# Performance work log

Hardware: AMD Instinct MI355X
Metric: run time of the kernel (lower is better)

Reference implementation:

```python
import jax, jax.numpy as jnp
import numpy as np


def setup_inputs() -> dict:
    key = jax.random.key(0)
    k0, k1, k2, k3 = jax.random.split(key, 4)
    B, s, D, E, H = 4, 1024, 1024, 8, 4096
    return {
        "x": jax.random.normal(k0, (B, s, D), dtype=jnp.float32),
        "gate_weight": jax.random.normal(k1, (E, D), dtype=jnp.float32) * 0.006,
        "expert_bias": jnp.zeros((E, 1), dtype=jnp.float32),
        "w1": jax.random.normal(k2, (E, D, H), dtype=jnp.float32) * 0.02,
        "b1": jnp.zeros((E, H), dtype=jnp.float32),
        "w2": jax.random.normal(k3, (E, H, D), dtype=jnp.float32) * 0.02,
        "b2": jnp.zeros((E, D), dtype=jnp.float32),
        "capacity": 2,
    }


def reference(x, gate_weight, expert_bias, w1, b1, w2, b2, capacity):
    B, s, D = x.shape
    E = gate_weight.shape[0]
    xf = x.reshape(-1, D)          # [S, D]
    S = xf.shape[0]
    k = int(S * capacity)          # number of routed (expert, token) pairs

    # Router: logits [E, S], softmax over experts (dim=0 in the torch code)
    logits = jnp.einsum('ed,sd->es', gate_weight, xf) + expert_bias
    scores = jax.nn.softmax(logits, axis=0)  # [E, S]

    # Global top-k over the flattened [E, S] score matrix (idx // S = expert,
    # idx % S = token, matching the source's index arithmetic).
    _, idx = jax.lax.top_k(scores.reshape(-1), k)
    sel = jnp.zeros((E * S,), dtype=scores.dtype).at[idx].set(1.0)
    combine = scores * sel.reshape(E, S)     # gating value where selected, else 0

    # Dense per-expert MLP on all tokens (same math as gather -> expert -> scatter,
    # expressed as masked combine). GELU(tanh approx) as in the repo's Mlp.
    h = jax.nn.gelu(jnp.einsum('sd,edh->esh', xf, w1) + b1[:, None, :],
                    approximate=True)        # [E, S, H]
    out_e = jnp.einsum('esh,ehd->esd', h, w2) + b2[:, None, :]  # [E, S, D]

    out = jnp.einsum('es,esd->sd', combine, out_e)  # scatter-combine
    return out.reshape(B, s, D)
```

## Files before the change

### kernel.cpp

```cpp
#include <hip/hip_runtime.h>
#include <stdint.h>

#define S_TOK 4096
#define DIM   1024
#define NE    8
#define HID   4096

typedef __attribute__((ext_vector_type(4))) float f32x4;
typedef __attribute__((ext_vector_type(8))) short bf16x8;

static __device__ __forceinline__ ushort f2bf(float f) {
  uint u = __float_as_uint(f);
  u += 0x7FFFu + ((u >> 16) & 1u);
  return (ushort)(u >> 16);
}

static __device__ __forceinline__ double shfl_xor_d(double v, int off) {
  long long l = __double_as_longlong(v);
  int lo = (int)(l & 0xFFFFFFFFll), hi = (int)(l >> 32);
  lo = __shfl_xor(lo, off);
  hi = __shfl_xor(hi, off);
  return __longlong_as_double(((long long)hi << 32) | (unsigned int)lo);
}

__global__ __launch_bounds__(256) void router_kernel(
    const float* __restrict__ x, const float* __restrict__ gw,
    const float* __restrict__ bias, double* __restrict__ scoresd,
    ushort* __restrict__ xb)
{
  const int t = blockIdx.x * 4 + (threadIdx.x >> 6);
  const int lane = threadIdx.x & 63;
  double acc[NE];
#pragma unroll
  for (int e = 0; e < NE; ++e) acc[e] = 0.0;
  const float4* xrow = (const float4*)(x + (size_t)t * DIM);
  ushort* xbrow = xb + (size_t)t * DIM;
#pragma unroll
  for (int j = 0; j < 4; ++j) {
    const int c4 = j * 64 + lane;
    float4 xv = xrow[c4];
    ushort4 bv;
    bv.x = f2bf(xv.x); bv.y = f2bf(xv.y); bv.z = f2bf(xv.z); bv.w = f2bf(xv.w);
    ((ushort4*)xbrow)[c4] = bv;
#pragma unroll
    for (int e = 0; e < NE; ++e) {
      float4 g = ((const float4*)(gw + (size_t)e * DIM))[c4];
      acc[e] += (double)xv.x * g.x + (double)xv.y * g.y
              + (double)xv.z * g.z + (double)xv.w * g.w;
    }
  }
#pragma unroll
  for (int e = 0; e < NE; ++e) {
    double v = acc[e];
#pragma unroll
    for (int off = 32; off >= 1; off >>= 1) v += shfl_xor_d(v, off);
    acc[e] = v + (double)bias[e];
  }
  double m = acc[0];
#pragma unroll
  for (int e = 1; e < NE; ++e) m = (acc[e] > m) ? acc[e] : m;
  double den = 0.0;
#pragma unroll
  for (int e = 0; e < NE; ++e) { acc[e] = exp(acc[e] - m); den += acc[e]; }
  const double inv = 1.0 / den;
#pragma unroll
  for (int e = 0; e < NE; ++e)
    if (lane == e) scoresd[(size_t)e * S_TOK + t] = acc[e] * inv;
}

__global__ __launch_bounds__(1024) void select_kernel(
    const double* __restrict__ scoresd, const int* __restrict__ capacity,
    int* __restrict__ counts, int* __restrict__ bases,
    int* __restrict__ lists, float* __restrict__ gates)
{
  __shared__ int sh_cnt;
  __shared__ unsigned long long sh_p;
  __shared__ int sh_r;
  __shared__ int wsum[16];
  __shared__ int sh_run;
  __shared__ int cnt_e[NE];
  const int tid = threadIdx.x, lane = tid & 63, wv = tid >> 6;
  const int k = S_TOK * capacity[0];

  unsigned long long key[32];
#pragma unroll
  for (int c = 0; c < 32; ++c)
    key[c] = (unsigned long long)__double_as_longlong(scoresd[c * 1024 + tid]);

  if (tid == 0) { sh_p = 0ull; sh_r = k; sh_run = 0; }
  if (tid < NE) cnt_e[tid] = 0;
  __syncthreads();

  for (int b = 63; b >= 0; --b) {
    if (tid == 0) sh_cnt = 0;
    __syncthreads();
    const unsigned long long p = sh_p;
    const unsigned long long mask = (~0ull) << b;
    const unsigned long long test = p | (1ull << b);
    int local = 0;
#pragma unroll
    for (int c = 0; c < 32; ++c) local += ((key[c] & mask) == test) ? 1 : 0;
#pragma unroll
    for (int off = 32; off >= 1; off >>= 1) local += __shfl_xor(local, off);
    if (lane == 0) atomicAdd(&sh_cnt, local);
    __syncthreads();
    if (tid == 0) {
      if (sh_r <= sh_cnt) sh_p |= (1ull << b); else sh_r -= sh_cnt;
    }
    __syncthreads();
  }
  const unsigned long long p = sh_p;

  if (tid == 0) sh_cnt = 0;
  __syncthreads();
  {
    int local = 0;
#pragma unroll
    for (int c = 0; c < 32; ++c) local += (key[c] > p) ? 1 : 0;
#pragma unroll
    for (int off = 32; off >= 1; off >>= 1) local += __shfl_xor(local, off);
    if (lane == 0) atomicAdd(&sh_cnt, local);
  }
  __syncthreads();
  const int need_eq = k - sh_cnt;

#pragma unroll
  for (int c = 0; c < 32; ++c) {
    const int i = c * 1024 + tid;
    const bool gt = key[c] > p;
    const bool eq = (key[c] == p);
    const unsigned long long bal = __ballot(eq);
    const int wpref = __popcll(bal & ((1ull << lane) - 1ull));
    if (lane == 0) wsum[wv] = __popcll(bal);
    __syncthreads();
    int wbase = 0;
    for (int w = 0; w < wv; ++w) wbase += wsum[w];
    const int rank = sh_run + wbase + wpref;
    if (gt || (eq && rank < need_eq)) {
      const int e = i >> 12;
      const int s = i & (S_TOK - 1);
      const int slot = atomicAdd(&cnt_e[e], 1);
      lists[e * S_TOK + slot] = s;
      gates[e * S_TOK + slot] = (float)__longlong_as_double((long long)key[c]);
    }
    __syncthreads();
    if (tid == 0) {
      int tot = 0;
      for (int w = 0; w < 16; ++w) tot += wsum[w];
      sh_run += tot;
    }
    __syncthreads();
  }

  if (tid == 0) {
    int b0 = 0;
    for (int e = 0; e < NE; ++e) { counts[e] = cnt_e[e]; bases[e] = b0; b0 += cnt_e[e]; }
  }
}

__global__ __launch_bounds__(256) void gemm1_kernel(
    const ushort* __restrict__ xb, const float* __restrict__ w1,
    const float* __restrict__ b1, const int* __restrict__ counts,
    const int* __restrict__ bases, const int* __restrict__ lists,
    ushort* __restrict__ hbuf)
{
  const int e = blockIdx.z;
  const int ne = counts[e];
  const int row0 = blockIdx.y * 128;
  if (row0 >= ne) return;
  const int n0 = blockIdx.x * 128;
  const int base = bases[e];

  __shared__ ushort Al[128 * 40];
  __shared__ ushort Bl[128 * 40];

  const int tid = threadIdx.x, lane = tid & 63, wid = tid >> 6;
  const int wm = wid >> 1, wn = wid & 1;

  const int ar0 = tid >> 2, ksa = tid & 3;
  const int tr0 = min(row0 + ar0, ne - 1);
  const int tr1 = min(row0 + 64 + ar0, ne - 1);
  const ushort* aptr0 = xb + (size_t)lists[e * S_TOK + tr0] * DIM + ksa * 8;
  const ushort* aptr1 = xb + (size_t)lists[e * S_TOK + tr1] * DIM + ksa * 8;

  const int hb = tid & 127, ksb = tid >> 7;
  const float* wb = w1 + (size_t)e * DIM * HID + (size_t)(n0 + hb);

  f32x4 acc[4][4];
#pragma unroll
  for (int i = 0; i < 4; ++i)
#pragma unroll
    for (int j = 0; j < 4; ++j) acc[i][j] = (f32x4){0.f, 0.f, 0.f, 0.f};

  for (int kk = 0; kk < DIM; kk += 32) {
    int4 av0 = *(const int4*)(aptr0 + kk);
    int4 av1 = *(const int4*)(aptr1 + kk);
    float fa[8], fbv[8];
#pragma unroll
    for (int j = 0; j < 8; ++j) {
      fa[j]  = wb[(size_t)(kk + ksb * 8 + j) * HID];
      fbv[j] = wb[(size_t)(kk + (ksb + 2) * 8 + j) * HID];
    }
    union { ushort u[8]; int4 v; } p0, p1;
#pragma unroll
    for (int j = 0; j < 8; ++j) { p0.u[j] = f2bf(fa[j]); p1.u[j] = f2bf(fbv[j]); }
    __syncthreads();
    *(int4*)&Al[ar0 * 40 + ksa * 8] = av0;
    *(int4*)&Al[(64 + ar0) * 40 + ksa * 8] = av1;
    *(int4*)&Bl[hb * 40 + ksb * 8] = p0.v;
    *(int4*)&Bl[hb * 40 + (ksb + 2) * 8] = p1.v;
    __syncthreads();
    bf16x8 af[4], bf[4];
#pragma unroll
    for (int m = 0; m < 4; ++m)
      af[m] = *(const bf16x8*)&Al[(wm * 64 + m * 16 + (lane & 15)) * 40 + (lane >> 4) * 8];
#pragma unroll
    for (int n = 0; n < 4; ++n)
      bf[n] = *(const bf16x8*)&Bl[(wn * 64 + n * 16 + (lane & 15)) * 40 + (lane >> 4) * 8];
#pragma unroll
    for (int m = 0; m < 4; ++m)
#pragma unroll
      for (int n = 0; n < 4; ++n)
        acc[m][n] = __builtin_amdgcn_mfma_f32_16x16x32_bf16(af[m], bf[n], acc[m][n], 0, 0, 0);
  }

  const float* b1e = b1 + (size_t)e * HID + n0;
#pragma unroll
  for (int m = 0; m < 4; ++m) {
#pragma unroll
    for (int r = 0; r < 4; ++r) {
      const int row = wm * 64 + m * 16 + (lane >> 4) * 4 + r;
      if (row0 + row < ne) {
        const size_t hrow = (size_t)(base + row0 + row) * HID + n0;
#pragma unroll
        for (int n = 0; n < 4; ++n) {
          const int col = wn * 64 + n * 16 + (lane & 15);
          float v = acc[m][n][r] + b1e[col];
          float t = v + 0.044715f * v * v * v;
          float g = v / (1.0f + __expf(-1.5957691216f * t));
          hbuf[hrow + col] = f2bf(g);
        }
      }
    }
  }
}

__global__ __launch_bounds__(256) void gemm2_kernel(
    const ushort* __restrict__ hbuf, const float* __restrict__ w2,
    const float* __restrict__ b2, const int* __restrict__ counts,
    const int* __restrict__ bases, const int* __restrict__ lists,
    const float* __restrict__ gates, float* __restrict__ out)
{
  const int e = blockIdx.z;
  const int ne = counts[e];
  const int row0 = blockIdx.y * 128;
  if (row0 >= ne) return;
  const int n0 = blockIdx.x * 128;
  const int base = bases[e];

  __shared__ ushort Al[128 * 40];
  __shared__ ushort Bl[128 * 40];

  const int tid = threadIdx.x, lane = tid & 63, wid = tid >> 6;
  const int wm = wid >> 1, wn = wid & 1;

  const int ar0 = tid >> 2, ksa = tid & 3;
  const size_t hr0 = (size_t)(base + min(row0 + ar0, ne - 1)) * HID;
  const size_t hr1 = (size_t)(base + min(row0 + 64 + ar0, ne - 1)) * HID;
  const ushort* aptr0 = hbuf + hr0 + ksa * 8;
  const ushort* aptr1 = hbuf + hr1 + ksa * 8;

  const int hb = tid & 127, ksb = tid >> 7;
  const float* wb = w2 + (size_t)e * HID * DIM + (size_t)(n0 + hb);

  f32x4 acc[4][4];
#pragma unroll
  for (int i = 0; i < 4; ++i)
#pragma unroll
    for (int j = 0; j < 4; ++j) acc[i][j] = (f32x4){0.f, 0.f, 0.f, 0.f};

  for (int kk = 0; kk < HID; kk += 32) {
    int4 av0 = *(const int4*)(aptr0 + kk);
    int4 av1 = *(const int4*)(aptr1 + kk);
    float fa[8], fbv[8];
#pragma unroll
    for (int j = 0; j < 8; ++j) {
      fa[j]  = wb[(size_t)(kk + ksb * 8 + j) * DIM];
      fbv[j] = wb[(size_t)(kk + (ksb + 2) * 8 + j) * DIM];
    }
    union { ushort u[8]; int4 v; } p0, p1;
#pragma unroll
    for (int j = 0; j < 8; ++j) { p0.u[j] = f2bf(fa[j]); p1.u[j] = f2bf(fbv[j]); }
    __syncthreads();
    *(int4*)&Al[ar0 * 40 + ksa * 8] = av0;
    *(int4*)&Al[(64 + ar0) * 40 + ksa * 8] = av1;
    *(int4*)&Bl[hb * 40 + ksb * 8] = p0.v;
    *(int4*)&Bl[hb * 40 + (ksb + 2) * 8] = p1.v;
    __syncthreads();
    bf16x8 af[4], bf[4];
#pragma unroll
    for (int m = 0; m < 4; ++m)
      af[m] = *(const bf16x8*)&Al[(wm * 64 + m * 16 + (lane & 15)) * 40 + (lane >> 4) * 8];
#pragma unroll
    for (int n = 0; n < 4; ++n)
      bf[n] = *(const bf16x8*)&Bl[(wn * 64 + n * 16 + (lane & 15)) * 40 + (lane >> 4) * 8];
#pragma unroll
    for (int m = 0; m < 4; ++m)
#pragma unroll
      for (int n = 0; n < 4; ++n)
        acc[m][n] = __builtin_amdgcn_mfma_f32_16x16x32_bf16(af[m], bf[n], acc[m][n], 0, 0, 0);
  }

  const float* b2e = b2 + (size_t)e * DIM + n0;
#pragma unroll
  for (int m = 0; m < 4; ++m) {
#pragma unroll
    for (int r = 0; r < 4; ++r) {
      const int row = wm * 64 + m * 16 + (lane >> 4) * 4 + r;
      if (row0 + row < ne) {
        const int tok = lists[e * S_TOK + row0 + row];
        const float gv = gates[e * S_TOK + row0 + row];
        float* orow = out + (size_t)tok * DIM + n0;
#pragma unroll
        for (int n = 0; n < 4; ++n) {
          const int col = wn * 64 + n * 16 + (lane & 15);
          const float v = gv * (acc[m][n][r] + b2e[col]);
          __hip_atomic_fetch_add(&orow[col], v, __ATOMIC_RELAXED, __HIP_MEMORY_SCOPE_AGENT);
        }
      }
    }
  }
}

extern "C" void kernel_launch(void* const* d_in, const int* in_sizes, int n_in,
                              void* d_out, int out_size, void* d_ws, size_t ws_size,
                              hipStream_t stream)
{
  const float* x    = (const float*)d_in[0];
  const float* gw   = (const float*)d_in[1];
  const float* bias = (const float*)d_in[2];
  const float* w1   = (const float*)d_in[3];
  const float* b1   = (const float*)d_in[4];
  const float* w2   = (const float*)d_in[5];
  const float* b2   = (const float*)d_in[6];
  const int*   cap  = (const int*)d_in[7];
  float* out = (float*)d_out;
  char* ws = (char*)d_ws;

  ushort* xb      = (ushort*)(ws);
  ushort* hbuf    = (ushort*)(ws + (size_t)8  * (1 << 20));
  double* scoresd = (double*)(ws + (size_t)72 * (1 << 20));
  int*    lists   = (int*)   (ws + (size_t)73 * (1 << 20));
  float*  gates   = (float*) (ws + (size_t)74 * (1 << 20));
  int*    counts  = (int*)   (ws + (size_t)75 * (1 << 20));
  int*    bases   = counts + 64;

  hipMemsetAsync(d_out, 0, (size_t)out_size * sizeof(float), stream);

  router_kernel<<<dim3(S_TOK / 4), 256, 0, stream>>>(x, gw, bias, scoresd, xb);
  select_kernel<<<dim3(1), 1024, 0, stream>>>(scoresd, cap, counts, bases, lists, gates);
  gemm1_kernel<<<dim3(HID / 128, 32, NE), 256, 0, stream>>>(xb, w1, b1, counts, bases, lists, hbuf);
  gemm2_kernel<<<dim3(DIM / 128, 32, NE), 256, 0, stream>>>(hbuf, w2, b2, counts, bases, lists, gates, out);
}
```

Baseline: 788.7 us.

## Pre-transpose weights to bf16 and stream tiles via global_load_lds in hidden chunks

Adds a per-call kernel that transposes and converts each expert's fp32 W1/W2 to bf16 in a K-contiguous layout. The GEMMs then load both operands with direct global-to-LDS 16-byte loads into a swizzled 32-wide LDS layout, replacing strided scalar fp32 weight loads and in-loop conversion. The hidden dimension is split into two chunks so the transposed weights and intermediate activations fit the workspace, and gemm2 accumulates each chunk atomically, adding the bias only once. The cost is extra weight-prep passes, more launches, and a second round of atomic output adds.

```diff
diff --git a/kernel.cpp b/kernel.cpp
--- a/kernel.cpp
+++ b/kernel.cpp
@@ -5,6 +5,7 @@
 #define DIM   1024
 #define NE    8
 #define HID   4096
+#define HC    2048
 
 typedef __attribute__((ext_vector_type(4))) float f32x4;
 typedef __attribute__((ext_vector_type(8))) short bf16x8;
@@ -13,6 +14,12 @@
   uint u = __float_as_uint(f);
   u += 0x7FFFu + ((u >> 16) & 1u);
   return (ushort)(u >> 16);
+}
+
+static __device__ __forceinline__ void gload16(const ushort* g, ushort* l) {
+  __builtin_amdgcn_global_load_lds(
+      (const __attribute__((address_space(1))) void*)g,
+      (__attribute__((address_space(3))) void*)l, 16, 0, 0);
 }
 
 static __device__ __forceinline__ double shfl_xor_d(double v, int off) {
@@ -21,6 +28,38 @@
   lo = __shfl_xor(lo, off);
   hi = __shfl_xor(hi, off);
   return __longlong_as_double(((long long)hi << 32) | (unsigned int)lo);
+}
+
+__global__ __launch_bounds__(256) void wprep_kernel(
+    const float* __restrict__ w, ushort* __restrict__ wT,
+    int R, int rowStride, size_t eIn, size_t eOut)
+{
+  __shared__ float tile[64][65];
+  const int e = blockIdx.z;
+  const int c0 = blockIdx.x * 64, r0 = blockIdx.y * 64;
+  const float* we = w + (size_t)e * eIn;
+  ushort* wTe = wT + (size_t)e * eOut;
+  const int t = threadIdx.x;
+  const int rr = t >> 4, cq = t & 15;
+#pragma unroll
+  for (int p = 0; p < 4; ++p) {
+    float4 v = *(const float4*)(we + (size_t)(r0 + p * 16 + rr) * rowStride + c0 + cq * 4);
+    tile[p * 16 + rr][cq * 4 + 0] = v.x;
+    tile[p * 16 + rr][cq * 4 + 1] = v.y;
+    tile[p * 16 + rr][cq * 4 + 2] = v.z;
+    tile[p * 16 + rr][cq * 4 + 3] = v.w;
+  }
+  __syncthreads();
+#pragma unroll
+  for (int p = 0; p < 4; ++p) {
+    const int cc = p * 16 + rr;
+    ushort4 o;
+    o.x = f2bf(tile[cq * 4 + 0][cc]);
+    o.y = f2bf(tile[cq * 4 + 1][cc]);
+    o.z = f2bf(tile[cq * 4 + 2][cc]);
+    o.w = f2bf(tile[cq * 4 + 3][cc]);
+    *(ushort4*)(wTe + (size_t)(c0 + cc) * R + r0 + cq * 4) = o;
+  }
 }
 
 __global__ __launch_bounds__(256) void router_kernel(
@@ -159,10 +198,10 @@
 }
 
 __global__ __launch_bounds__(256) void gemm1_kernel(
-    const ushort* __restrict__ xb, const float* __restrict__ w1,
+    const ushort* __restrict__ xb, const ushort* __restrict__ wT,
     const float* __restrict__ b1, const int* __restrict__ counts,
     const int* __restrict__ bases, const int* __restrict__ lists,
-    ushort* __restrict__ hbuf)
+    ushort* __restrict__ hbuf, int hc0)
 {
   const int e = blockIdx.z;
   const int ne = counts[e];
@@ -171,20 +210,28 @@
   const int n0 = blockIdx.x * 128;
   const int base = bases[e];
 
-  __shared__ ushort Al[128 * 40];
-  __shared__ ushort Bl[128 * 40];
-
-  const int tid = threadIdx.x, lane = tid & 63, wid = tid >> 6;
-  const int wm = wid >> 1, wn = wid & 1;
-
-  const int ar0 = tid >> 2, ksa = tid & 3;
-  const int tr0 = min(row0 + ar0, ne - 1);
-  const int tr1 = min(row0 + 64 + ar0, ne - 1);
-  const ushort* aptr0 = xb + (size_t)lists[e * S_TOK + tr0] * DIM + ksa * 8;
-  const ushort* aptr1 = xb + (size_t)lists[e * S_TOK + tr1] * DIM + ksa * 8;
-
-  const int hb = tid & 127, ksb = tid >> 7;
-  const float* wb = w1 + (size_t)e * DIM * HID + (size_t)(n0 + hb);
+  __shared__ ushort Al[128 * 32];
+  __shared__ ushort Bl[128 * 32];
+
+  const int tid = threadIdx.x, lane = tid & 63, w = tid >> 6;
+  const int wm = w >> 1, wn = w & 1;
+  const int r15 = lane & 15;
+
+  const int sr = w * 32 + (lane >> 2);
+  const int sslot = (lane & 3) ^ ((lane >> 3) & 3);
+  const int tr0 = min(row0 + sr, ne - 1);
+  const int tr1 = min(row0 + sr + 16, ne - 1);
+  const ushort* ap0 = xb + (size_t)lists[e * S_TOK + tr0] * DIM + sslot * 8;
+  const ushort* ap1 = xb + (size_t)lists[e * S_TOK + tr1] * DIM + sslot * 8;
+  const ushort* wTe = wT + (size_t)e * HC * DIM;
+  const ushort* bp0 = wTe + (size_t)(n0 + sr) * DIM + sslot * 8;
+  const ushort* bp1 = wTe + (size_t)(n0 + sr + 16) * DIM + sslot * 8;
+  ushort* la0 = &Al[w * 1024];
+  ushort* la1 = &Al[w * 1024 + 512];
+  ushort* lb0 = &Bl[w * 1024];
+  ushort* lb1 = &Bl[w * 1024 + 512];
+
+  const int slotr = ((lane >> 4) ^ ((lane >> 1) & 3)) * 8;
 
   f32x4 acc[4][4];
 #pragma unroll
@@ -193,48 +240,37 @@
     for (int j = 0; j < 4; ++j) acc[i][j] = (f32x4){0.f, 0.f, 0.f, 0.f};
 
   for (int kk = 0; kk < DIM; kk += 32) {
-    int4 av0 = *(const int4*)(aptr0 + kk);
-    int4 av1 = *(const int4*)(aptr1 + kk);
-    float fa[8], fbv[8];
-#pragma unroll
-    for (int j = 0; j < 8; ++j) {
-      fa[j]  = wb[(size_t)(kk + ksb * 8 + j) * HID];
-      fbv[j] = wb[(size_t)(kk + (ksb + 2) * 8 + j) * HID];
-    }
-    union { ushort u[8]; int4 v; } p0, p1;
-#pragma unroll
-    for (int j = 0; j < 8; ++j) { p0.u[j] = f2bf(fa[j]); p1.u[j] = f2bf(fbv[j]); }
-    __syncthreads();
-    *(int4*)&Al[ar0 * 40 + ksa * 8] = av0;
-    *(int4*)&Al[(64 + ar0) * 40 + ksa * 8] = av1;
-    *(int4*)&Bl[hb * 40 + ksb * 8] = p0.v;
-    *(int4*)&Bl[hb * 40 + (ksb + 2) * 8] = p1.v;
-    __syncthreads();
-    bf16x8 af[4], bf[4];
+    __syncthreads();
+    gload16(ap0 + kk, la0);
+    gload16(ap1 + kk, la1);
+    gload16(bp0 + kk, lb0);
+    gload16(bp1 + kk, lb1);
+    __syncthreads();
+    bf16x8 af[4], bfr[4];
 #pragma unroll
     for (int m = 0; m < 4; ++m)
-      af[m] = *(const bf16x8*)&Al[(wm * 64 + m * 16 + (lane & 15)) * 40 + (lane >> 4) * 8];
+      af[m] = *(const bf16x8*)&Al[(wm * 64 + m * 16 + r15) * 32 + slotr];
 #pragma unroll
     for (int n = 0; n < 4; ++n)
-      bf[n] = *(const bf16x8*)&Bl[(wn * 64 + n * 16 + (lane & 15)) * 40 + (lane >> 4) * 8];
+      bfr[n] = *(const bf16x8*)&Bl[(wn * 64 + n * 16 + r15) * 32 + slotr];
 #pragma unroll
     for (int m = 0; m < 4; ++m)
 #pragma unroll
       for (int n = 0; n < 4; ++n)
-        acc[m][n] = __builtin_amdgcn_mfma_f32_16x16x32_bf16(af[m], bf[n], acc[m][n], 0, 0, 0);
-  }
-
-  const float* b1e = b1 + (size_t)e * HID + n0;
+        acc[m][n] = __builtin_amdgcn_mfma_f32_16x16x32_bf16(af[m], bfr[n], acc[m][n], 0, 0, 0);
+  }
+
+  const float* b1e = b1 + (size_t)e * HID + hc0 + n0;
 #pragma unroll
   for (int m = 0; m < 4; ++m) {
 #pragma unroll
     for (int r = 0; r < 4; ++r) {
       const int row = wm * 64 + m * 16 + (lane >> 4) * 4 + r;
       if (row0 + row < ne) {
-        const size_t hrow = (size_t)(base + row0 + row) * HID + n0;
+        const size_t hrow = (size_t)(base + row0 + row) * HC + n0;
 #pragma unroll
         for (int n = 0; n < 4; ++n) {
-          const int col = wn * 64 + n * 16 + (lane & 15);
+          const int col = wn * 64 + n * 16 + r15;
           float v = acc[m][n][r] + b1e[col];
           float t = v + 0.044715f * v * v * v;
           float g = v / (1.0f + __expf(-1.5957691216f * t));
@@ -246,10 +282,10 @@
 }
 
 __global__ __launch_bounds__(256) void gemm2_kernel(
-    const ushort* __restrict__ hbuf, const float* __restrict__ w2,
+    const ushort* __restrict__ hbuf, const ushort* __restrict__ wT,
     const float* __restrict__ b2, const int* __restrict__ counts,
     const int* __restrict__ bases, const int* __restrict__ lists,
-    const float* __restrict__ gates, float* __restrict__ out)
+    const float* __restrict__ gates, float* __restrict__ out, int addBias)
 {
   const int e = blockIdx.z;
   const int ne = counts[e];
@@ -258,20 +294,28 @@
   const int n0 = blockIdx.x * 128;
   const int base = bases[e];
 
-  __shared__ ushort Al[128 * 40];
-  __shared__ ushort Bl[128 * 40];
-
-  const int tid = threadIdx.x, lane = tid & 63, wid = tid >> 6;
-  const int wm = wid >> 1, wn = wid & 1;
-
-  const int ar0 = tid >> 2, ksa = tid & 3;
-  const size_t hr0 = (size_t)(base + min(row0 + ar0, ne - 1)) * HID;
-  const size_t hr1 = (size_t)(base + min(row0 + 64 + ar0, ne - 1)) * HID;
-  const ushort* aptr0 = hbuf + hr0 + ksa * 8;
-  const ushort* aptr1 = hbuf + hr1 + ksa * 8;
-
-  const int hb = tid & 127, ksb = tid >> 7;
-  const float* wb = w2 + (size_t)e * HID * DIM + (size_t)(n0 + hb);
+  __shared__ ushort Al[128 * 32];
+  __shared__ ushort Bl[128 * 32];
+
+  const int tid = threadIdx.x, lane = tid & 63, w = tid >> 6;
+  const int wm = w >> 1, wn = w & 1;
+  const int r15 = lane & 15;
+
+  const int sr = w * 32 + (lane >> 2);
+  const int sslot = (lane & 3) ^ ((lane >> 3) & 3);
+  const int tr0 = min(row0 + sr, ne - 1);
+  const int tr1 = min(row0 + sr + 16, ne - 1);
+  const ushort* ap0 = hbuf + (size_t)(base + tr0) * HC + sslot * 8;
+  const ushort* ap1 = hbuf + (size_t)(base + tr1) * HC + sslot * 8;
+  const ushort* wTe = wT + (size_t)e * DIM * HC;
+  const ushort* bp0 = wTe + (size_t)(n0 + sr) * HC + sslot * 8;
+  const ushort* bp1 = wTe + (size_t)(n0 + sr + 16) * HC + sslot * 8;
+  ushort* la0 = &Al[w * 1024];
+  ushort* la1 = &Al[w * 1024 + 512];
+  ushort* lb0 = &Bl[w * 1024];
+  ushort* lb1 = &Bl[w * 1024 + 512];
+
+  const int slotr = ((lane >> 4) ^ ((lane >> 1) & 3)) * 8;
 
   f32x4 acc[4][4];
 #pragma unroll
@@ -279,36 +323,25 @@
 #pragma unroll
     for (int j = 0; j < 4; ++j) acc[i][j] = (f32x4){0.f, 0.f, 0.f, 0.f};
 
-  for (int kk = 0; kk < HID; kk += 32) {
-    int4 av0 = *(const int4*)(aptr0 + kk);
-    int4 av1 = *(const int4*)(aptr1 + kk);
-    float fa[8], fbv[8];
-#pragma unroll
-    for (int j = 0; j < 8; ++j) {
-      fa[j]  = wb[(size_t)(kk + ksb * 8 + j) * DIM];
-      fbv[j] = wb[(size_t)(kk + (ksb + 2) * 8 + j) * DIM];
-    }
-    union { ushort u[8]; int4 v; } p0, p1;
-#pragma unroll
-    for (int j = 0; j < 8; ++j) { p0.u[j] = f2bf(fa[j]); p1.u[j] = f2bf(fbv[j]); }
-    __syncthreads();
-    *(int4*)&Al[ar0 * 40 + ksa * 8] = av0;
-    *(int4*)&Al[(64 + ar0) * 40 + ksa * 8] = av1;
-    *(int4*)&Bl[hb * 40 + ksb * 8] = p0.v;
-    *(int4*)&Bl[hb * 40 + (ksb + 2) * 8] = p1.v;
-    __syncthreads();
-    bf16x8 af[4], bf[4];
+  for (int kk = 0; kk < HC; kk += 32) {
+    __syncthreads();
+    gload16(ap0 + kk, la0);
+    gload16(ap1 + kk, la1);
+    gload16(bp0 + kk, lb0);
+    gload16(bp1 + kk, lb1);
+    __syncthreads();
+    bf16x8 af[4], bfr[4];
 #pragma unroll
     for (int m = 0; m < 4; ++m)
-      af[m] = *(const bf16x8*)&Al[(wm * 64 + m * 16 + (lane & 15)) * 40 + (lane >> 4) * 8];
+      af[m] = *(const bf16x8*)&Al[(wm * 64 + m * 16 + r15) * 32 + slotr];
 #pragma unroll
     for (int n = 0; n < 4; ++n)
-      bf[n] = *(const bf16x8*)&Bl[(wn * 64 + n * 16 + (lane & 15)) * 40 + (lane >> 4) * 8];
+      bfr[n] = *(const bf16x8*)&Bl[(wn * 64 + n * 16 + r15) * 32 + slotr];
 #pragma unroll
     for (int m = 0; m < 4; ++m)
 #pragma unroll
       for (int n = 0; n < 4; ++n)
-        acc[m][n] = __builtin_amdgcn_mfma_f32_16x16x32_bf16(af[m], bf[n], acc[m][n], 0, 0, 0);
+        acc[m][n] = __builtin_amdgcn_mfma_f32_16x16x32_bf16(af[m], bfr[n], acc[m][n], 0, 0, 0);
   }
 
   const float* b2e = b2 + (size_t)e * DIM + n0;
@@ -323,8 +356,9 @@
         float* orow = out + (size_t)tok * DIM + n0;
 #pragma unroll
         for (int n = 0; n < 4; ++n) {
-          const int col = wn * 64 + n * 16 + (lane & 15);
-          const float v = gv * (acc[m][n][r] + b2e[col]);
+          const int col = wn * 64 + n * 16 + r15;
+          const float bb = addBias ? b2e[col] : 0.f;
+          const float v = gv * (acc[m][n][r] + bb);
           __hip_atomic_fetch_add(&orow[col], v, __ATOMIC_RELAXED, __HIP_MEMORY_SCOPE_AGENT);
         }
       }
@@ -349,16 +383,27 @@
 
   ushort* xb      = (ushort*)(ws);
   ushort* hbuf    = (ushort*)(ws + (size_t)8  * (1 << 20));
+  ushort* wT      = (ushort*)(ws + (size_t)40 * (1 << 20));
   double* scoresd = (double*)(ws + (size_t)72 * (1 << 20));
-  int*    lists   = (int*)   (ws + (size_t)73 * (1 << 20));
-  float*  gates   = (float*) (ws + (size_t)74 * (1 << 20));
-  int*    counts  = (int*)   (ws + (size_t)75 * (1 << 20));
+  int*    lists   = (int*)   (ws + (size_t)72 * (1 << 20) + 262144);
+  float*  gates   = (float*) (ws + (size_t)72 * (1 << 20) + 262144 + 131072);
+  int*    counts  = (int*)   (ws + (size_t)72 * (1 << 20) + 262144 + 262144);
   int*    bases   = counts + 64;
 
   hipMemsetAsync(d_out, 0, (size_t)out_size * sizeof(float), stream);
 
   router_kernel<<<dim3(S_TOK / 4), 256, 0, stream>>>(x, gw, bias, scoresd, xb);
   select_kernel<<<dim3(1), 1024, 0, stream>>>(scoresd, cap, counts, bases, lists, gates);
-  gemm1_kernel<<<dim3(HID / 128, 32, NE), 256, 0, stream>>>(xb, w1, b1, counts, bases, lists, hbuf);
-  gemm2_kernel<<<dim3(DIM / 128, 32, NE), 256, 0, stream>>>(hbuf, w2, b2, counts, bases, lists, gates, out);
-}
+
+  for (int chunk = 0; chunk < 2; ++chunk) {
+    const int hc0 = chunk * HC;
+    wprep_kernel<<<dim3(HC / 64, DIM / 64, NE), 256, 0, stream>>>(
+        w1 + hc0, wT, DIM, HID, (size_t)DIM * HID, (size_t)HC * DIM);
+    gemm1_kernel<<<dim3(HC / 128, 32, NE), 256, 0, stream>>>(
+        xb, wT, b1, counts, bases, lists, hbuf, hc0);
+    wprep_kernel<<<dim3(DIM / 64, HC / 64, NE), 256, 0, stream>>>(
+        w2 + (size_t)hc0 * DIM, wT, HC, DIM, (size_t)HID * DIM, (size_t)DIM * HC);
+    gemm2_kernel<<<dim3(DIM / 128, 32, NE), 256, 0, stream>>>(
+        hbuf, wT, b2, counts, bases, lists, gates, out, chunk == 0 ? 1 : 0);
+  }
+}
```

Measured after the change: 744.8 us. -5.6%, faster.
